# Kernel optimization log

Measured on AMD Instinct MI355X. Metric: run time of the kernel, lower is better.

The kernel has to match this reference:

```python
import jax, jax.numpy as jnp
import numpy as np

B, C, H, W, NP = 4, 512, 32, 32, 2048
NH = 4
EPS = 1e-5


def setup_inputs() -> dict:
    key = jax.random.key(0)
    ks = jax.random.split(key, 12)
    s = 0.02
    d = {}
    d["img_feature"] = jax.random.normal(ks[0], (B, C, H, W), jnp.float32)
    d["point_feature"] = jax.random.normal(ks[1], (B, C, NP), jnp.float32)
    d["mlp_w1"] = jax.random.normal(ks[2], (2 * C, C), jnp.float32) * s
    d["mlp_b1"] = jnp.zeros((2 * C,), jnp.float32)
    d["bn1_gamma"] = jnp.ones((2 * C,), jnp.float32)
    d["bn1_beta"] = jnp.zeros((2 * C,), jnp.float32)
    d["bn1_mean"] = jnp.zeros((2 * C,), jnp.float32)
    d["bn1_var"] = jnp.ones((2 * C,), jnp.float32)
    d["mlp_w2"] = jax.random.normal(ks[3], (C, 2 * C), jnp.float32) * s
    d["mlp_b2"] = jnp.zeros((C,), jnp.float32)
    d["bn2_gamma"] = jnp.ones((C,), jnp.float32)
    d["bn2_beta"] = jnp.zeros((C,), jnp.float32)
    d["bn2_mean"] = jnp.zeros((C,), jnp.float32)
    d["bn2_var"] = jnp.ones((C,), jnp.float32)
    d["attn_qw"] = jax.random.normal(ks[4], (3, C, C), jnp.float32) * s
    d["attn_qb"] = jnp.zeros((3, C), jnp.float32)
    d["attn_kw"] = jax.random.normal(ks[5], (3, C, C), jnp.float32) * s
    d["attn_kb"] = jnp.zeros((3, C), jnp.float32)
    d["attn_vw"] = jax.random.normal(ks[6], (3, C, C), jnp.float32) * s
    d["attn_vb"] = jnp.zeros((3, C), jnp.float32)
    d["attn_ln_g"] = jnp.ones((3, C), jnp.float32)
    d["attn_ln_b"] = jnp.zeros((3, C), jnp.float32)
    return d


def _bn(x, g, b, m, v):  # x: [B, C, N], eval-mode batchnorm over channel dim
    return (x - m[:, None]) * jax.lax.rsqrt(v[:, None] + EPS) * g[:, None] + b[:, None]


def _mlp(x, w1, b1, g1, be1, m1, v1, w2, b2, g2, be2, m2, v2):
    # 1x1 Conv1d == per-position linear over channels
    y = jnp.einsum('oc,bcn->bon', w1, x) + b1[:, None]
    y = jax.nn.relu(_bn(y, g1, be1, m1, v1))
    z = jnp.einsum('oc,bcn->bon', w2, y) + b2[:, None]
    return jax.nn.relu(_bn(z, g2, be2, m2, v2))


def _self_attn(x, qw, qb, kw, kb, vw, vb, lng, lnb):
    # x: [B, S, E]; NOTE: original scales by 1/sqrt(hidden_size), not head_dim
    Bq, S, E = x.shape
    Hd = E // NH
    q = (jnp.einsum('bse,de->bsd', x, qw) + qb).reshape(Bq, S, NH, Hd)
    k = (jnp.einsum('bse,de->bsd', x, kw) + kb).reshape(Bq, S, NH, Hd)
    v = (jnp.einsum('bse,de->bsd', x, vw) + vb).reshape(Bq, S, NH, Hd)
    scores = jnp.einsum('bqhd,bkhd->bhqk', q, k) * (float(E) ** -0.5)
    attn = jax.nn.softmax(scores, axis=-1)
    out = jnp.einsum('bhqk,bkhd->bqhd', attn, v).reshape(Bq, S, E)
    y = out + x
    mu = jnp.mean(y, axis=-1, keepdims=True)
    var = jnp.var(y, axis=-1, keepdims=True)
    return (y - mu) * jax.lax.rsqrt(var + EPS) * lng + lnb


def reference(img_feature, point_feature, mlp_w1, mlp_b1, bn1_gamma, bn1_beta,
              bn1_mean, bn1_var, mlp_w2, mlp_b2, bn2_gamma, bn2_beta, bn2_mean,
              bn2_var, attn_qw, attn_qb, attn_kw, attn_kb, attn_vw, attn_vb,
              attn_ln_g, attn_ln_b):
    b, c, h, w = img_feature.shape
    i_in = img_feature.reshape(b, c, h * w)  # [B, C, N_i]
    mlp_args = (mlp_w1, mlp_b1, bn1_gamma, bn1_beta, bn1_mean, bn1_var,
                mlp_w2, mlp_b2, bn2_gamma, bn2_beta, bn2_mean, bn2_var)
    p_feat = _mlp(point_feature, *mlp_args)  # [B, C, N_p]
    i_feat = _mlp(i_in, *mlp_args)           # [B, C, N_i]
    phi = jnp.einsum('bcp,bci->bpi', p_feat, i_feat) * (float(c) ** -0.5)
    phi_p = jax.nn.softmax(phi, axis=1)   # softmax over points
    phi_i = jax.nn.softmax(phi, axis=-1)  # softmax over image positions
    I_enh = jnp.einsum('bcp,bpi->bci', p_feat, phi_p)  # [B, C, N_i]
    P_enh = jnp.einsum('bci,bpi->bcp', i_feat, phi_i)  # [B, C, N_p]
    att = lambda x, j: _self_attn(x, attn_qw[j], attn_qb[j], attn_kw[j],
                                  attn_kb[j], attn_vw[j], attn_vb[j],
                                  attn_ln_g[j], attn_ln_b[j])
    I = att(jnp.swapaxes(I_enh, 1, 2), 0)  # [B, N_i, C]
    P = att(jnp.swapaxes(P_enh, 1, 2), 1)  # [B, N_p, C]
    joint = jnp.concatenate([P, I], axis=1)  # [B, N_p + N_i, C]
    return att(joint, 2)
```

## Files before the change

### kernel.cpp

```cpp
#include <hip/hip_runtime.h>
#include <math.h>

#define LN_EPS 1e-5f

typedef __attribute__((ext_vector_type(8))) short bf16x8;
typedef __attribute__((ext_vector_type(4))) float f32x4;

#define GLDS16(g, l) __builtin_amdgcn_global_load_lds( \
    (const __attribute__((address_space(1))) unsigned int*)(g), \
    (__attribute__((address_space(3))) unsigned int*)(l), 16, 0, 0)

__device__ __forceinline__ float b2f(unsigned short h) { return __uint_as_float(((unsigned)h) << 16); }
__device__ __forceinline__ unsigned short f2b(float f) {
  unsigned u = __float_as_uint(f);
  unsigned r = (u + 0x7fffu + ((u >> 16) & 1u)) >> 16;
  return (unsigned short)r;
}
__device__ __forceinline__ float ld(const float* p) { return *p; }
__device__ __forceinline__ float ld(const unsigned short* p) { return b2f(*p); }
__device__ __forceinline__ void st(float* p, float v) { *p = v; }
__device__ __forceinline__ void st(unsigned short* p, float v) { *p = f2b(v); }

__device__ __forceinline__ float bred_sum(float v, float* red) {
  for (int o = 32; o; o >>= 1) v += __shfl_down(v, o, 64);
  int wid = threadIdx.x >> 6;
  __syncthreads();
  if ((threadIdx.x & 63) == 0) red[wid] = v;
  __syncthreads();
  return red[0] + red[1] + red[2] + red[3];
}

__global__ void fold_bn(const float* b1, const float* g1, const float* be1,
                        const float* m1, const float* v1,
                        const float* b2, const float* g2, const float* be2,
                        const float* m2, const float* v2,
                        float* s1, float* f1, float* s2, float* f2) {
  int t = blockIdx.x * 256 + threadIdx.x;
  if (t < 1024) { float s = g1[t] * rsqrtf(v1[t] + LN_EPS); s1[t] = s; f1[t] = (b1[t] - m1[t]) * s + be1[t]; }
  if (t < 512)  { float s = g2[t] * rsqrtf(v2[t] + LN_EPS); s2[t] = s; f2[t] = (b2[t] - m2[t]) * s + be2[t]; }
}

__global__ void cvt_bf16(const float* __restrict__ s, unsigned short* __restrict__ d, int n) {
  int i = blockIdx.x * 256 + threadIdx.x;
  if (i < n) d[i] = f2b(s[i]);
}

__global__ void prep_qk(const float* __restrict__ qw, const float* __restrict__ qb,
                        const float* __restrict__ kw, const float* __restrict__ kb,
                        unsigned short* __restrict__ qkw, float* __restrict__ qkbias) {
  const float scl = 0.044194173824159216f;
  int idx = blockIdx.x * 256 + threadIdx.x;
  if (idx < 1572864) {
    int j = idx >> 19; int r = idx & 524287; int n = r >> 9; int k = r & 511;
    float v = (n < 512) ? qw[j * 262144 + n * 512 + k] * scl
                        : kw[j * 262144 + (n - 512) * 512 + k];
    qkw[idx] = f2b(v);
  }
  if (idx < 3072) {
    int j = idx >> 10, n = idx & 1023;
    qkbias[idx] = (n < 512) ? qb[j * 512 + n] * scl : kb[j * 512 + n - 512];
  }
}

template<typename TS, typename TD>
__global__ __launch_bounds__(256) void transpose_t(const TS* __restrict__ src,
    TD* __restrict__ dst, int R, int Cc, long sS, long sD) {
  __shared__ float t[32][33];
  src += (long)blockIdx.z * sS; dst += (long)blockIdx.z * sD;
  int c0 = blockIdx.x * 32, r0 = blockIdx.y * 32;
  int tx = threadIdx.x & 31, ty = threadIdx.x >> 5;
#pragma unroll
  for (int rr = 0; rr < 32; rr += 8) t[ty + rr][tx] = ld(&src[(long)(r0 + ty + rr) * Cc + c0 + tx]);
  __syncthreads();
#pragma unroll
  for (int rr = 0; rr < 32; rr += 8) st(&dst[(long)(c0 + ty + rr) * R + r0 + tx], t[tx][ty + rr]);
}

template<int PER>
__global__ __launch_bounds__(256) void softmax_k(const float* __restrict__ x,
    unsigned short* __restrict__ y, long bstr) {
  __shared__ float red[4];
  const int L = PER * 256;
  int b = blockIdx.y, r = blockIdx.x, tid = threadIdx.x;
  const float* p = x + (long)b * bstr + (long)r * L;
  unsigned short* o = y + (long)b * bstr + (long)r * L;
  float vals[PER];
  float mx = -1e30f;
#pragma unroll
  for (int t = 0; t < PER; t++) { float v = p[tid + (t << 8)]; vals[t] = v; mx = fmaxf(mx, v); }
  for (int ofs = 32; ofs; ofs >>= 1) mx = fmaxf(mx, __shfl_down(mx, ofs, 64));
  int wid = tid >> 6;
  if ((tid & 63) == 0) red[wid] = mx;
  __syncthreads();
  mx = fmaxf(fmaxf(red[0], red[1]), fmaxf(red[2], red[3]));
  float sm = 0.f;
#pragma unroll
  for (int t = 0; t < PER; t++) { float e = __expf(vals[t] - mx); vals[t] = e; sm += e; }
  sm = bred_sum(sm, red);
  float inv = 1.f / sm;
#pragma unroll
  for (int t = 0; t < PER; t++) o[tid + (t << 8)] = f2b(vals[t] * inv);
}

template<int EPI, typename TC>
__global__ __launch_bounds__(256) void gemm_bf16(
    const unsigned short* __restrict__ A, long sA, int lda,
    const unsigned short* __restrict__ B, long sB, int ldb,
    TC* __restrict__ C, long sC, int ldc,
    int M, int N, int K,
    const float* __restrict__ sc, const float* __restrict__ bi, float cscale)
{
  __shared__ short As[128 * 64];
  __shared__ short Bs[128 * 64];
  const int tid = threadIdx.x;
  const int lane = tid & 63, wid = tid >> 6;
  const int wm = wid >> 1, wn = wid & 1;
  const int l15 = lane & 15, l4 = lane >> 4, l7 = lane & 7;
  const int bm = blockIdx.y * 128, bn = blockIdx.x * 128;
  const int srow = lane >> 3;
  A += (long)blockIdx.z * sA; B += (long)blockIdx.z * sB; C += (long)blockIdx.z * sC;
  f32x4 acc[4][4] = {};
  for (int k0 = 0; k0 < K; k0 += 64) {
#pragma unroll
    for (int i = 0; i < 4; i++) {
      int row = (wid * 4 + i) * 8 + srow;
      int gcol = (l7 ^ (row & 7)) * 8;
      GLDS16(A + (long)(bm + row) * lda + k0 + gcol, &As[(wid * 4 + i) * 512]);
      GLDS16(B + (long)(bn + row) * ldb + k0 + gcol, &Bs[(wid * 4 + i) * 512]);
    }
    __syncthreads();
#pragma unroll
    for (int ks = 0; ks < 2; ks++) {
      bf16x8 af[4], bfr[4];
#pragma unroll
      for (int t = 0; t < 4; t++) {
        int ra = wm * 64 + t * 16 + l15;
        int rb = wn * 64 + t * 16 + l15;
        int ch = (l4 + 4 * ks) ^ (l15 & 7);
        af[t]  = *(const bf16x8*)&As[ra * 64 + ch * 8];
        bfr[t] = *(const bf16x8*)&Bs[rb * 64 + ch * 8];
      }
#pragma unroll
      for (int i = 0; i < 4; i++)
#pragma unroll
        for (int j2 = 0; j2 < 4; j2++)
          acc[i][j2] = __builtin_amdgcn_mfma_f32_16x16x32_bf16(af[i], bfr[j2], acc[i][j2], 0, 0, 0);
    }
    __syncthreads();
  }
#pragma unroll
  for (int i = 0; i < 4; i++) {
#pragma unroll
    for (int j2 = 0; j2 < 4; j2++) {
      int n = bn + wn * 64 + j2 * 16 + l15;
#pragma unroll
      for (int j = 0; j < 4; j++) {
        int m = bm + wm * 64 + i * 16 + l4 * 4 + j;
        float v = acc[i][j2][j];
        if (EPI == 1) v = fmaxf(fmaf(v, sc[n], bi[n]), 0.f);
        if (EPI == 2) v *= cscale;
        if (EPI == 3) v += bi[n];
        if (EPI == 4) v += bi[m];
        st(&C[(long)m * ldc + n], v);
      }
    }
  }
}

__global__ __launch_bounds__(512) void attn_flash(
    const unsigned short* __restrict__ qk, const unsigned short* __restrict__ vT,
    float* __restrict__ out, int S)
{
  __shared__ short Ks[2][64 * 128];
  __shared__ short Vs[2][128 * 64];
  __shared__ short Ps[8][1024];
  const int tid = threadIdx.x, lane = tid & 63, wid = tid >> 6;
  const int h = blockIdx.y, b = blockIdx.z;
  const int l15 = lane & 15, l4 = lane >> 4, l7 = l15 & 7;
  const long qkb = (long)b * S * 1024;
  const long vbb = (long)b * 512 * S;
  const long obase = (long)b * S * 512;
  const int qr0 = blockIdx.x * 128 + wid * 16;
  bf16x8 qf[4];
#pragma unroll
  for (int ks = 0; ks < 4; ks++)
    qf[ks] = *(const bf16x8*)(qk + qkb + (long)(qr0 + l15) * 1024 + h * 128 + l4 * 8 + ks * 32);
  f32x4 O[8] = {};
  float m_run = -1e30f, l_run = 0.f;
  const int NT = S >> 6;
  auto stage = [&](int bi, int kt) {
#pragma unroll
    for (int i = 0; i < 2; i++) {
      int krow = wid * 8 + i * 4 + (lane >> 4);
      GLDS16(qk + qkb + (long)(kt * 64 + krow) * 1024 + 512 + h * 128 + (((lane & 15) ^ (krow & 7)) << 3),
             &Ks[bi][(wid * 8 + i * 4) * 128]);
      int vrow = wid * 16 + i * 8 + (lane >> 3);
      GLDS16(vT + vbb + (long)(h * 128 + vrow) * S + kt * 64 + (((lane & 7) ^ (vrow & 7)) << 3),
             &Vs[bi][(wid * 16 + i * 8) * 64]);
    }
  };
  stage(0, 0);
  int cur = 0;
  for (int kt = 0; kt < NT; kt++) {
    __syncthreads();
    if (kt + 1 < NT) stage(cur ^ 1, kt + 1);
    f32x4 sacc[4] = {};
    __builtin_amdgcn_s_setprio(1);
#pragma unroll
    for (int f = 0; f < 4; f++) {
      int row = f * 16 + l15;
#pragma unroll
      for (int ks = 0; ks < 4; ks++) {
        bf16x8 kf = *(const bf16x8*)&Ks[cur][row * 128 + (((l4 + 4 * ks) ^ l7) << 3)];
        sacc[f] = __builtin_amdgcn_mfma_f32_16x16x32_bf16(kf, qf[ks], sacc[f], 0, 0, 0);
      }
    }
    __builtin_amdgcn_s_setprio(0);
    float pmax = -1e30f;
#pragma unroll
    for (int f = 0; f < 4; f++)
#pragma unroll
      for (int j = 0; j < 4; j++) pmax = fmaxf(pmax, sacc[f][j]);
    pmax = fmaxf(pmax, __shfl_xor(pmax, 16, 64));
    pmax = fmaxf(pmax, __shfl_xor(pmax, 32, 64));
    if (!__all(pmax - m_run <= 8.f)) {
      float m_new = fmaxf(m_run, pmax);
      float corr = __expf(m_run - m_new);
      l_run *= corr; m_run = m_new;
#pragma unroll
      for (int fd = 0; fd < 8; fd++) {
        O[fd][0] *= corr; O[fd][1] *= corr; O[fd][2] *= corr; O[fd][3] *= corr;
      }
    }
    float ts = 0.f;
#pragma unroll
    for (int f = 0; f < 4; f++) {
      ushort4 pw;
#pragma unroll
      for (int j = 0; j < 4; j++) {
        float e = __expf(sacc[f][j] - m_run);
        ts += e;
        ((unsigned short*)&pw)[j] = f2b(e);
      }
      *(ushort4*)&Ps[wid][l15 * 64 + (((2 * f + (l4 >> 1)) ^ l7) << 3) + (l4 & 1) * 4] = pw;
    }
    ts += __shfl_xor(ts, 16, 64);
    ts += __shfl_xor(ts, 32, 64);
    l_run += ts;
    __builtin_amdgcn_s_setprio(1);
#pragma unroll
    for (int ks = 0; ks < 2; ks++) {
      int pch = ((l4 + 4 * ks) ^ l7) << 3;
      bf16x8 pf = *(const bf16x8*)&Ps[wid][l15 * 64 + pch];
#pragma unroll
      for (int fd = 0; fd < 8; fd++) {
        bf16x8 vf = *(const bf16x8*)&Vs[cur][(fd * 16 + l15) * 64 + pch];
        O[fd] = __builtin_amdgcn_mfma_f32_16x16x32_bf16(vf, pf, O[fd], 0, 0, 0);
      }
    }
    __builtin_amdgcn_s_setprio(0);
    cur ^= 1;
  }
  float inv = 1.f / l_run;
  float* op = out + obase + (long)(qr0 + l15) * 512 + h * 128;
#pragma unroll
  for (int fd = 0; fd < 8; fd++) {
    f32x4 ov = O[fd];
    ov[0] *= inv; ov[1] *= inv; ov[2] *= inv; ov[3] *= inv;
    *(f32x4*)&op[fd * 16 + l4 * 4] = ov;
  }
}

template<typename TD>
__global__ __launch_bounds__(256) void add_ln(
    const float* __restrict__ att, const unsigned short* __restrict__ resid,
    const float* __restrict__ g, const float* __restrict__ bt,
    TD* __restrict__ dst, long db, int S)
{
  __shared__ float red[4];
  int b = blockIdx.y, s = blockIdx.x, tid = threadIdx.x;
  const float* ap = att + ((long)b * S + s) * 512;
  const unsigned short* rp = resid + ((long)b * S + s) * 512;
  float y0 = ap[tid] + b2f(rp[tid]);
  float y1 = ap[tid + 256] + b2f(rp[tid + 256]);
  float mu = bred_sum(y0 + y1, red) * (1.f / 512.f);
  float d0 = y0 - mu, d1 = y1 - mu;
  float var = bred_sum(d0 * d0 + d1 * d1, red) * (1.f / 512.f);
  float rsv = rsqrtf(var + LN_EPS);
  TD* dp = dst + (long)b * db + (long)s * 512;
  st(&dp[tid], d0 * rsv * g[tid] + bt[tid]);
  st(&dp[tid + 256], d1 * rsv * g[tid + 256] + bt[tid + 256]);
}

extern "C" void kernel_launch(void* const* d_in, const int* in_sizes, int n_in,
                              void* d_out, int out_size, void* d_ws, size_t ws_size,
                              hipStream_t stream) {
  (void)in_sizes; (void)n_in; (void)out_size; (void)ws_size;
  const float* img = (const float*)d_in[0];
  const float* pts = (const float*)d_in[1];
  const float* w1  = (const float*)d_in[2];
  const float* b1  = (const float*)d_in[3];
  const float* g1  = (const float*)d_in[4];
  const float* be1 = (const float*)d_in[5];
  const float* m1  = (const float*)d_in[6];
  const float* v1  = (const float*)d_in[7];
  const float* w2  = (const float*)d_in[8];
  const float* b2  = (const float*)d_in[9];
  const float* g2  = (const float*)d_in[10];
  const float* be2 = (const float*)d_in[11];
  const float* m2  = (const float*)d_in[12];
  const float* v2  = (const float*)d_in[13];
  const float* qw  = (const float*)d_in[14];
  const float* qb  = (const float*)d_in[15];
  const float* kw  = (const float*)d_in[16];
  const float* kb  = (const float*)d_in[17];
  const float* vw  = (const float*)d_in[18];
  const float* vb  = (const float*)d_in[19];
  const float* lng = (const float*)d_in[20];
  const float* lnb = (const float*)d_in[21];
  float* out = (float*)d_out;
  float* ws  = (float*)d_ws;
  typedef unsigned short u16;

  u16*   xTu   = (u16*)ws;
  float* phi   = ws;
  u16*   y1u   = (u16*)(ws + 8388608);
  float* phiT  = ws + 8388608;
  u16*   featu = (u16*)(ws + 16777216);
  u16*   featTu= (u16*)(ws + 19922944);
  u16*   smI   = (u16*)(ws + 23068672);
  u16*   smPT  = (u16*)(ws + 27262976);
  u16*   Xi    = (u16*)(ws + 31457280);
  u16*   Xp    = (u16*)(ws + 32505856);
  u16*   jointu= (u16*)(ws + 34603008);
  u16*   w1b   = (u16*)(ws + 37748736);
  u16*   w2b   = (u16*)(ws + 38010880);
  u16*   qkwb  = (u16*)(ws + 38273024);
  u16*   vwb   = (u16*)(ws + 39059456);
  float* s1f   = ws + 39452672;
  float* f1f   = s1f + 1024;
  float* s2f   = f1f + 1024;
  float* f2f   = s2f + 512;
  float* qkbf  = ws + 39455744;
  u16*   qkbu  = (u16*)ws;
  u16*   vTu   = (u16*)(ws + 6291456);
  float* attf  = ws + 9437184;

  dim3 blk(256);
  fold_bn<<<dim3(4), blk, 0, stream>>>(b1, g1, be1, m1, v1, b2, g2, be2, m2, v2, s1f, f1f, s2f, f2f);
  cvt_bf16<<<dim3(2048), blk, 0, stream>>>(w1, w1b, 524288);
  cvt_bf16<<<dim3(2048), blk, 0, stream>>>(w2, w2b, 524288);
  cvt_bf16<<<dim3(3072), blk, 0, stream>>>(vw, vwb, 786432);
  prep_qk<<<dim3(6144), blk, 0, stream>>>(qw, qb, kw, kb, qkwb, qkbf);

  transpose_t<float, u16><<<dim3(64, 16, 4), blk, 0, stream>>>(pts, xTu, 512, 2048, 1048576L, 1572864L);
  transpose_t<float, u16><<<dim3(32, 16, 4), blk, 0, stream>>>(img, xTu + 1048576, 512, 1024, 524288L, 1572864L);

  gemm_bf16<1, u16><<<dim3(8, 24, 4), blk, 0, stream>>>(xTu, 1572864L, 512, w1b, 0L, 512,
      y1u, 3145728L, 1024, 3072, 1024, 512, s1f, f1f, 0.f);
  gemm_bf16<1, u16><<<dim3(4, 24, 4), blk, 0, stream>>>(y1u, 3145728L, 1024, w2b, 0L, 1024,
      featu, 1572864L, 512, 3072, 512, 1024, s2f, f2f, 0.f);
  transpose_t<u16, u16><<<dim3(16, 96, 4), blk, 0, stream>>>(featu, featTu, 3072, 512, 1572864L, 1572864L);
  gemm_bf16<2, float><<<dim3(8, 16, 4), blk, 0, stream>>>(featu, 1572864L, 512, featu + 1048576, 1572864L, 512,
      phi, 2097152L, 1024, 2048, 1024, 512, nullptr, nullptr, 0.044194173824159216f);
  transpose_t<float, float><<<dim3(32, 64, 4), blk, 0, stream>>>(phi, phiT, 2048, 1024, 2097152L, 2097152L);
  softmax_k<4><<<dim3(2048, 4), blk, 0, stream>>>(phi, smI, 2097152L);
  softmax_k<8><<<dim3(1024, 4), blk, 0, stream>>>(phiT, smPT, 2097152L);
  gemm_bf16<0, u16><<<dim3(4, 8, 4), blk, 0, stream>>>(smPT, 2097152L, 2048, featTu, 1572864L, 3072,
      Xi, 524288L, 512, 1024, 512, 2048, nullptr, nullptr, 0.f);
  gemm_bf16<0, u16><<<dim3(4, 16, 4), blk, 0, stream>>>(smI, 2097152L, 1024, featTu + 2048, 1572864L, 3072,
      Xp, 1048576L, 512, 2048, 512, 1024, nullptr, nullptr, 0.f);

  struct AttCfg { const u16* X; int S; int j; };
  AttCfg cfgs[3] = { {Xi, 1024, 0}, {Xp, 2048, 1}, {jointu, 3072, 2} };
  for (int a = 0; a < 3; a++) {
    const u16* X = cfgs[a].X; int S = cfgs[a].S; int j = cfgs[a].j;
    long xs = (long)S * 512;
    gemm_bf16<3, u16><<<dim3(8, S / 128, 4), blk, 0, stream>>>(X, xs, 512, qkwb + j * 524288, 0L, 512,
        qkbu, (long)S * 1024, 1024, S, 1024, 512, nullptr, qkbf + j * 1024, 0.f);
    gemm_bf16<4, u16><<<dim3(S / 128, 4, 4), blk, 0, stream>>>(vwb + j * 262144, 0L, 512, X, xs, 512,
        vTu, xs, S, 512, S, 512, nullptr, vb + j * 512, 0.f);
    attn_flash<<<dim3(S / 128, 4, 4), dim3(512), 0, stream>>>(qkbu, vTu, attf, S);
    if (a == 0)
      add_ln<u16><<<dim3(S, 4), blk, 0, stream>>>(attf, X, lng + j * 512, lnb + j * 512,
          jointu + 1048576, 1572864L, S);
    else if (a == 1)
      add_ln<u16><<<dim3(S, 4), blk, 0, stream>>>(attf, X, lng + j * 512, lnb + j * 512,
          jointu, 1572864L, S);
    else
      add_ln<float><<<dim3(S, 4), blk, 0, stream>>>(attf, X, lng + j * 512, lnb + j * 512,
          out, 1572864L, S);
  }
}
```

Before: 552.0 us.

## Stage K/V tiles through registers into single LDS buffer in flash attention

```diff
diff --git a/kernel.cpp b/kernel.cpp
--- a/kernel.cpp
+++ b/kernel.cpp
@@ -167,12 +167,12 @@
   }
 }
 
-__global__ __launch_bounds__(512) void attn_flash(
+__global__ __launch_bounds__(512, 6) void attn_flash(
     const unsigned short* __restrict__ qk, const unsigned short* __restrict__ vT,
     float* __restrict__ out, int S)
 {
-  __shared__ short Ks[2][64 * 128];
-  __shared__ short Vs[2][128 * 64];
+  __shared__ short Ks[64 * 128];
+  __shared__ short Vs[128 * 64];
   __shared__ short Ps[8][1024];
   const int tid = threadIdx.x, lane = tid & 63, wid = tid >> 6;
   const int h = blockIdx.y, b = blockIdx.z;
@@ -181,6 +181,11 @@
   const long vbb = (long)b * 512 * S;
   const long obase = (long)b * S * 512;
   const int qr0 = blockIdx.x * 128 + wid * 16;
+  const int ck0 = tid, ck1 = tid + 512;
+  const int kR0 = ck0 >> 4, kC0 = ck0 & 15;
+  const int kR1 = ck1 >> 4, kC1 = ck1 & 15;
+  const int vR0 = ck0 >> 3, vC0 = ck0 & 7;
+  const int vR1 = ck1 >> 3, vC1 = ck1 & 7;
   bf16x8 qf[4];
 #pragma unroll
   for (int ks = 0; ks < 4; ks++)
@@ -188,22 +193,22 @@
   f32x4 O[8] = {};
   float m_run = -1e30f, l_run = 0.f;
   const int NT = S >> 6;
-  auto stage = [&](int bi, int kt) {
-#pragma unroll
-    for (int i = 0; i < 2; i++) {
-      int krow = wid * 8 + i * 4 + (lane >> 4);
-      GLDS16(qk + qkb + (long)(kt * 64 + krow) * 1024 + 512 + h * 128 + (((lane & 15) ^ (krow & 7)) << 3),
-             &Ks[bi][(wid * 8 + i * 4) * 128]);
-      int vrow = wid * 16 + i * 8 + (lane >> 3);
-      GLDS16(vT + vbb + (long)(h * 128 + vrow) * S + kt * 64 + (((lane & 7) ^ (vrow & 7)) << 3),
-             &Vs[bi][(wid * 16 + i * 8) * 64]);
-    }
+  int4 kr0, kr1, vr0, vr1;
+  auto load_regs = [&](int kt) {
+    kr0 = *(const int4*)(qk + qkb + (long)(kt * 64 + kR0) * 1024 + 512 + h * 128 + kC0 * 8);
+    kr1 = *(const int4*)(qk + qkb + (long)(kt * 64 + kR1) * 1024 + 512 + h * 128 + kC1 * 8);
+    vr0 = *(const int4*)(vT + vbb + (long)(h * 128 + vR0) * S + kt * 64 + vC0 * 8);
+    vr1 = *(const int4*)(vT + vbb + (long)(h * 128 + vR1) * S + kt * 64 + vC1 * 8);
   };
-  stage(0, 0);
-  int cur = 0;
+  load_regs(0);
   for (int kt = 0; kt < NT; kt++) {
     __syncthreads();
-    if (kt + 1 < NT) stage(cur ^ 1, kt + 1);
+    *(int4*)&Ks[kR0 * 128 + ((kC0 ^ (kR0 & 7)) << 3)] = kr0;
+    *(int4*)&Ks[kR1 * 128 + ((kC1 ^ (kR1 & 7)) << 3)] = kr1;
+    *(int4*)&Vs[vR0 * 64 + ((vC0 ^ (vR0 & 7)) << 3)] = vr0;
+    *(int4*)&Vs[vR1 * 64 + ((vC1 ^ (vR1 & 7)) << 3)] = vr1;
+    __syncthreads();
+    if (kt + 1 < NT) load_regs(kt + 1);
     f32x4 sacc[4] = {};
     __builtin_amdgcn_s_setprio(1);
 #pragma unroll
@@ -211,7 +216,7 @@
       int row = f * 16 + l15;
 #pragma unroll
       for (int ks = 0; ks < 4; ks++) {
-        bf16x8 kf = *(const bf16x8*)&Ks[cur][row * 128 + (((l4 + 4 * ks) ^ l7) << 3)];
+        bf16x8 kf = *(const bf16x8*)&Ks[row * 128 + (((l4 + 4 * ks) ^ l7) << 3)];
         sacc[f] = __builtin_amdgcn_mfma_f32_16x16x32_bf16(kf, qf[ks], sacc[f], 0, 0, 0);
       }
     }
@@ -254,12 +259,11 @@
       bf16x8 pf = *(const bf16x8*)&Ps[wid][l15 * 64 + pch];
 #pragma unroll
       for (int fd = 0; fd < 8; fd++) {
-        bf16x8 vf = *(const bf16x8*)&Vs[cur][(fd * 16 + l15) * 64 + pch];
+        bf16x8 vf = *(const bf16x8*)&Vs[(fd * 16 + l15) * 64 + pch];
         O[fd] = __builtin_amdgcn_mfma_f32_16x16x32_bf16(vf, pf, O[fd], 0, 0, 0);
       }
     }
     __builtin_amdgcn_s_setprio(0);
-    cur ^= 1;
   }
   float inv = 1.f / l_run;
   float* op = out + obase + (long)(qr0 + l15) * 512 + h * 128;
```

Result: slower. 1.115 ms (+102.0%).
